# Performance work log

Hardware: AMD Instinct MI355X
Metric: run time of the kernel (lower is better)

The kernel has to match this reference:

```python
import jax, jax.numpy as jnp
import numpy as np

B, A, S, IN, H, OUT, T = 32768, 10, 50, 6, 64, 2, 60


def _p(key, shape, scale=0.1):
    return (jax.random.normal(key, shape) * scale).astype(jnp.float32)


def setup_inputs() -> dict:
    key = jax.random.key(0)
    ks = jax.random.split(key, 20)
    inp = {
        'history': jax.random.normal(ks[0], (B, A, S, IN), dtype=jnp.float32),
        # encoder layer 0 (IN->H) and layer 1 (H->H); PyTorch gate order i,f,g,o
        'enc_Wih0': _p(ks[1], (4 * H, IN)), 'enc_Whh0': _p(ks[2], (4 * H, H)),
        'enc_bih0': _p(ks[3], (4 * H,)),    'enc_bhh0': _p(ks[4], (4 * H,)),
        'enc_Wih1': _p(ks[5], (4 * H, H)),  'enc_Whh1': _p(ks[6], (4 * H, H)),
        'enc_bih1': _p(ks[7], (4 * H,)),    'enc_bhh1': _p(ks[8], (4 * H,)),
        # decoder layer 0 (OUT->H) and layer 1 (H->H)
        'dec_Wih0': _p(ks[9], (4 * H, OUT)), 'dec_Whh0': _p(ks[10], (4 * H, H)),
        'dec_bih0': _p(ks[11], (4 * H,)),    'dec_bhh0': _p(ks[12], (4 * H,)),
        'dec_Wih1': _p(ks[13], (4 * H, H)),  'dec_Whh1': _p(ks[14], (4 * H, H)),
        'dec_bih1': _p(ks[15], (4 * H,)),    'dec_bhh1': _p(ks[16], (4 * H,)),
        'lin_W': _p(ks[17], (OUT, H)), 'lin_b': _p(ks[18], (OUT,)),
        'start_token': _p(ks[19], (1, 1, OUT)),
    }
    return inp


def _cell(x, h, c, Wih, Whh, bih, bhh):
    g = x @ Wih.T + h @ Whh.T + (bih + bhh)
    i, f, gg, o = jnp.split(g, 4, axis=-1)
    c2 = jax.nn.sigmoid(f) * c + jax.nn.sigmoid(i) * jnp.tanh(gg)
    h2 = jax.nn.sigmoid(o) * jnp.tanh(c2)
    return h2, c2


def reference(history, enc_Wih0, enc_Whh0, enc_bih0, enc_bhh0,
              enc_Wih1, enc_Whh1, enc_bih1, enc_bhh1,
              dec_Wih0, dec_Whh0, dec_bih0, dec_bhh0,
              dec_Wih1, dec_Whh1, dec_bih1, dec_bhh1,
              lin_W, lin_b, start_token):
    ego = history[:, 0]                     # [B, S, IN]
    b = ego.shape[0]
    z = jnp.zeros((b, H), dtype=ego.dtype)

    def enc_step(carry, xt):
        h0, c0, h1, c1 = carry
        h0, c0 = _cell(xt, h0, c0, enc_Wih0, enc_Whh0, enc_bih0, enc_bhh0)
        h1, c1 = _cell(h0, h1, c1, enc_Wih1, enc_Whh1, enc_bih1, enc_bhh1)
        return (h0, c0, h1, c1), None

    (h0, c0, h1, c1), _ = jax.lax.scan(enc_step, (z, z, z, z),
                                       jnp.swapaxes(ego, 0, 1))  # time-major [S,B,IN]

    start = jnp.broadcast_to(start_token[0], (b, start_token.shape[2]))  # [B, OUT]

    def dec_step(carry, _):
        h0, c0, h1, c1, inp = carry
        h0, c0 = _cell(inp, h0, c0, dec_Wih0, dec_Whh0, dec_bih0, dec_bhh0)
        h1, c1 = _cell(h0, h1, c1, dec_Wih1, dec_Whh1, dec_bih1, dec_bhh1)
        out = h1 @ lin_W.T + lin_b           # [B, OUT]
        return (h0, c0, h1, c1, out), out

    _, preds = jax.lax.scan(dec_step, (h0, c0, h1, c1, start), None, length=T)
    return jnp.swapaxes(preds, 0, 1)         # [B, T, OUT]
```

## Files before the change

kernel.cpp:

```cpp
#include <hip/hip_runtime.h>
#include <stdint.h>

typedef float f32x4 __attribute__((ext_vector_type(4)));
typedef float f32x2 __attribute__((ext_vector_type(2)));
typedef __bf16 bf16x8 __attribute__((ext_vector_type(8)));
typedef __bf16 bf16x4 __attribute__((ext_vector_type(4)));

#define SEQ 50
#define TDEC 60

static __device__ __forceinline__ float ex2(float x){return __builtin_amdgcn_exp2f(x);}
static __device__ __forceinline__ float frcp_(float x){return __builtin_amdgcn_rcpf(x);}
static __device__ __forceinline__ __bf16 bfc(float x){return (__bf16)x;}

__global__ __launch_bounds__(256,2) void lstm_s2s(
    const float* __restrict__ hist,
    const float* __restrict__ eWih0, const float* __restrict__ eWhh0,
    const float* __restrict__ ebih0, const float* __restrict__ ebhh0,
    const float* __restrict__ eWih1, const float* __restrict__ eWhh1,
    const float* __restrict__ ebih1, const float* __restrict__ ebhh1,
    const float* __restrict__ dWih0, const float* __restrict__ dWhh0,
    const float* __restrict__ dbih0, const float* __restrict__ dbhh0,
    const float* __restrict__ dWih1, const float* __restrict__ dWhh1,
    const float* __restrict__ dbih1, const float* __restrict__ dbhh1,
    const float* __restrict__ linW, const float* __restrict__ linb,
    const float* __restrict__ stok,
    float* __restrict__ out)
{
  __shared__ __bf16 xch[SEQ*16*8];
  __shared__ __bf16 hb0[2][1024];
  __shared__ __bf16 hb1[2][1024];
  __shared__ __bf16 wx0s[4*4*17*8];
  __shared__ float  bC1[256];
  __shared__ __bf16 wlc[2*3*4*8];
  __shared__ float  obf[16*124];

  const int tid = threadIdx.x;
  const int lane = tid & 63;
  const int w = tid >> 6;
  const int c = lane & 15;
  const int q = lane >> 4;
  const int rsel = (q == 0) ? c : 16;
  const long rowbase = (long)blockIdx.x * 16;
  const float* eg = hist + rowbase * 3000;

  union { f32x4 f; bf16x8 h; } Z;
  Z.f[0]=0.f; Z.f[1]=0.f; Z.f[2]=0.f; Z.f[3]=0.f;
  const f32x4 zero4 = Z.f;
  const bf16x8 zfrag = Z.h;

  const float GS[4] = {-1.442695041f,-1.442695041f,2.885390082f,-1.442695041f};

  for (int i = tid; i < 16*300; i += 256) {
    int row = i / 300, o = i - row*300;
    int t = o / 6, k = o - t*6;
    xch[(t*16+row)*8 + k] = bfc(eg[row*3000 + o]);
  }
  for (int i = tid; i < 16*SEQ; i += 256) {
    xch[i*8+6] = (__bf16)1.0f;
    xch[i*8+7] = (__bf16)0.0f;
  }
  for (int i = tid; i < 512; i += 256) {
    ((uint32_t*)hb0[0])[i] = 0u;
    ((uint32_t*)hb1[0])[i] = 0u;
  }

  auto stageWx0 = [&](const float* W, int Kin, const float* bi, const float* bh) {
    for (int i = tid; i < 272; i += 256) {
      int w2 = i / 68, rem = i - w2*68;
      int g = rem / 17, row = rem - g*17;
      __bf16* dst = wx0s + i*8;
      if (row < 16) {
        int gate = (g*4 + w2)*16 + row;
        float gs = (g==2) ? 2.885390082f : -1.442695041f;
        for (int j = 0; j < 8; ++j) {
          float v = 0.f;
          if (j < Kin) v = W[gate*Kin + j];
          else if (j == 6) v = bi[gate] + bh[gate];
          dst[j] = bfc(gs*v);
        }
      } else {
        for (int j = 0; j < 8; ++j) dst[j] = (__bf16)0.f;
      }
    }
  };
  auto stageBc1 = [&](const float* bi, const float* bh) {
    for (int i = tid; i < 256; i += 256) {
      int w2 = i >> 6, g = (i >> 4) & 3, q2 = (i >> 2) & 3, r = i & 3;
      int gate = (g*4 + w2)*16 + q2*4 + r;
      float gs = (g==2) ? 2.885390082f : -1.442695041f;
      bC1[i] = gs*(bi[gate] + bh[gate]);
    }
  };

  bf16x8 whL0[4][2], wxL1[4][2], whL1[4][2];
  auto loadFull = [&](const float* W, bf16x8 (*dst)[2]) {
#pragma unroll
    for (int g = 0; g < 4; ++g)
#pragma unroll
      for (int kc = 0; kc < 2; ++kc) {
        const float* p = W + ((g*4 + w)*16 + c)*64 + kc*32 + q*8;
        f32x4 a = *(const f32x4*)p;
        f32x4 b = *(const f32x4*)(p + 4);
        bf16x8 f;
        f[0]=bfc(GS[g]*a[0]); f[1]=bfc(GS[g]*a[1]);
        f[2]=bfc(GS[g]*a[2]); f[3]=bfc(GS[g]*a[3]);
        f[4]=bfc(GS[g]*b[0]); f[5]=bfc(GS[g]*b[1]);
        f[6]=bfc(GS[g]*b[2]); f[7]=bfc(GS[g]*b[3]);
        dst[g][kc] = f;
      }
  };

  const int wconst = (w>>1)*512 + (((w&1)<<1) | (q>>1))*128 + c*8 + (q&1)*4;

  float cs0[4], cs1[4];
#pragma unroll
  for (int i = 0; i < 4; ++i) { cs0[i] = 0.f; cs1[i] = 0.f; }

  auto epilogue = [&](f32x4* a, float* cs, __bf16* hnxt) {
    bf16x4 hv;
#pragma unroll
    for (int r = 0; r < 4; ++r) {
      float eI = ex2(a[0][r]);
      float eF = ex2(a[1][r]);
      float eG = ex2(a[2][r]);
      float eO = ex2(a[3][r]);
      float P  = (1.f+eI)*(eG+1.f);
      float tt = 1.f+eF;
      float D  = frcp_(tt*P);
      float c2 = (cs[r]*P + (eG-1.f)*tt)*D;
      float eC = ex2(2.885390082f*c2);
      float h2 = (eC-1.f)*frcp_((1.f+eO)*(eC+1.f));
      cs[r] = c2;
      hv[r] = bfc(h2);
    }
    *(bf16x4*)(hnxt + wconst) = hv;
  };

  stageWx0(eWih0, 6, ebih0, ebhh0);
  stageBc1(ebih1, ebhh1);
  loadFull(eWhh0, whL0);
  loadFull(eWih1, wxL1);
  loadFull(eWhh1, whL1);
  __syncthreads();

  f32x4 acc0[4];
  {
    bf16x8 xf = zfrag;
    if (q == 0) xf = *(const bf16x8*)(xch + c*8);
#pragma unroll
    for (int g = 0; g < 4; ++g) {
      bf16x8 wxf = *(const bf16x8*)(wx0s + ((w*4+g)*17 + rsel)*8);
      acc0[g] = __builtin_amdgcn_mfma_f32_16x16x32_bf16(wxf, xf, zero4, 0,0,0);
    }
  }

  int pc = 0;
#pragma unroll 1
  for (int t = 0; t < SEQ; ++t) {
    f32x4 acc1[4];
    {
      const __bf16* h1p = hb1[pc];
      bf16x8 hf0 = *(const bf16x8*)(h1p + lane*8);
      bf16x8 hf1 = *(const bf16x8*)(h1p + 512 + lane*8);
#pragma unroll
      for (int g = 0; g < 4; ++g) {
        f32x4 bi4 = *(const f32x4*)(bC1 + w*64 + g*16 + q*4);
        acc1[g] = __builtin_amdgcn_mfma_f32_16x16x32_bf16(whL1[g][0], hf0, bi4, 0,0,0);
      }
#pragma unroll
      for (int g = 0; g < 4; ++g)
        acc1[g] = __builtin_amdgcn_mfma_f32_16x16x32_bf16(whL1[g][1], hf1, acc1[g], 0,0,0);
    }
    epilogue(acc0, cs0, hb0[pc^1]);
    __syncthreads();
    {
      const __bf16* h0n = hb0[pc^1];
      bf16x8 xf0 = *(const bf16x8*)(h0n + lane*8);
      bf16x8 xf1 = *(const bf16x8*)(h0n + 512 + lane*8);
#pragma unroll
      for (int g = 0; g < 4; ++g)
        acc1[g] = __builtin_amdgcn_mfma_f32_16x16x32_bf16(wxL1[g][0], xf0, acc1[g], 0,0,0);
#pragma unroll
      for (int g = 0; g < 4; ++g)
        acc1[g] = __builtin_amdgcn_mfma_f32_16x16x32_bf16(wxL1[g][1], xf1, acc1[g], 0,0,0);
      epilogue(acc1, cs1, hb1[pc^1]);
      if (t + 1 < SEQ) {
        bf16x8 xf = zfrag;
        if (q == 0) xf = *(const bf16x8*)(xch + (t+1)*128 + c*8);
#pragma unroll
        for (int g = 0; g < 4; ++g) {
          bf16x8 wxf = *(const bf16x8*)(wx0s + ((w*4+g)*17 + rsel)*8);
          acc0[g] = __builtin_amdgcn_mfma_f32_16x16x32_bf16(wxf, xf, zero4, 0,0,0);
        }
#pragma unroll
        for (int g = 0; g < 4; ++g)
          acc0[g] = __builtin_amdgcn_mfma_f32_16x16x32_bf16(whL0[g][0], xf0, acc0[g], 0,0,0);
#pragma unroll
        for (int g = 0; g < 4; ++g)
          acc0[g] = __builtin_amdgcn_mfma_f32_16x16x32_bf16(whL0[g][1], xf1, acc0[g], 0,0,0);
      }
    }
    __syncthreads();
    pc ^= 1;
  }

  stageWx0(dWih0, 2, dbih0, dbhh0);
  stageBc1(dbih1, dbhh1);
  loadFull(dWhh0, whL0);
  loadFull(dWih1, wxL1);
  loadFull(dWhh1, whL1);
  for (int i = tid; i < 24; i += 256) {
    int kc = i / 12, rem = i - kc*12;
    int row = rem / 4, q2 = rem - row*4;
    __bf16* dst = wlc + i*8;
    for (int j = 0; j < 8; ++j)
      dst[j] = (row < 2) ? bfc(linW[row*64 + kc*32 + q2*8 + j]) : (__bf16)0.f;
  }
  const float lb0 = linb[0], lb1 = linb[1];
  const float s0 = stok[0], s1 = stok[1];
  __syncthreads();

  bf16x8 xdec = zfrag;
  if (q == 0) { xdec[0] = bfc(s0); xdec[1] = bfc(s1); xdec[6] = (__bf16)1.0f; }
  {
    const __bf16* h0p = hb0[pc];
    bf16x8 hf0 = *(const bf16x8*)(h0p + lane*8);
    bf16x8 hf1 = *(const bf16x8*)(h0p + 512 + lane*8);
#pragma unroll
    for (int g = 0; g < 4; ++g) {
      bf16x8 wxf = *(const bf16x8*)(wx0s + ((w*4+g)*17 + rsel)*8);
      acc0[g] = __builtin_amdgcn_mfma_f32_16x16x32_bf16(wxf, xdec, zero4, 0,0,0);
    }
#pragma unroll
    for (int g = 0; g < 4; ++g)
      acc0[g] = __builtin_amdgcn_mfma_f32_16x16x32_bf16(whL0[g][0], hf0, acc0[g], 0,0,0);
#pragma unroll
    for (int g = 0; g < 4; ++g)
      acc0[g] = __builtin_amdgcn_mfma_f32_16x16x32_bf16(whL0[g][1], hf1, acc0[g], 0,0,0);
  }

#pragma unroll 1
  for (int t = 0; t < TDEC; ++t) {
    f32x4 acc1[4];
    {
      const __bf16* h1p = hb1[pc];
      bf16x8 hf0 = *(const bf16x8*)(h1p + lane*8);
      bf16x8 hf1 = *(const bf16x8*)(h1p + 512 + lane*8);
#pragma unroll
      for (int g = 0; g < 4; ++g) {
        f32x4 bi4 = *(const f32x4*)(bC1 + w*64 + g*16 + q*4);
        acc1[g] = __builtin_amdgcn_mfma_f32_16x16x32_bf16(whL1[g][0], hf0, bi4, 0,0,0);
      }
#pragma unroll
      for (int g = 0; g < 4; ++g)
        acc1[g] = __builtin_amdgcn_mfma_f32_16x16x32_bf16(whL1[g][1], hf1, acc1[g], 0,0,0);
    }
    epilogue(acc0, cs0, hb0[pc^1]);
    __syncthreads();
    {
      const __bf16* h0n = hb0[pc^1];
      bf16x8 xf0 = *(const bf16x8*)(h0n + lane*8);
      bf16x8 xf1 = *(const bf16x8*)(h0n + 512 + lane*8);
#pragma unroll
      for (int g = 0; g < 4; ++g)
        acc1[g] = __builtin_amdgcn_mfma_f32_16x16x32_bf16(wxL1[g][0], xf0, acc1[g], 0,0,0);
#pragma unroll
      for (int g = 0; g < 4; ++g)
        acc1[g] = __builtin_amdgcn_mfma_f32_16x16x32_bf16(wxL1[g][1], xf1, acc1[g], 0,0,0);
      epilogue(acc1, cs1, hb1[pc^1]);
      if (t + 1 < TDEC) {
#pragma unroll
        for (int g = 0; g < 4; ++g)
          acc0[g] = __builtin_amdgcn_mfma_f32_16x16x32_bf16(whL0[g][0], xf0, zero4, 0,0,0);
#pragma unroll
        for (int g = 0; g < 4; ++g)
          acc0[g] = __builtin_amdgcn_mfma_f32_16x16x32_bf16(whL0[g][1], xf1, acc0[g], 0,0,0);
      }
    }
    __syncthreads();
    {
      const __bf16* h1n = hb1[pc^1];
      bf16x8 xh0 = *(const bf16x8*)(h1n + lane*8);
      bf16x8 xh1 = *(const bf16x8*)(h1n + 512 + lane*8);
      int hr = (c < 2) ? c : 2;
      bf16x8 wl0 = *(const bf16x8*)(wlc + hr*32 + q*8);
      bf16x8 wl1 = *(const bf16x8*)(wlc + 96 + hr*32 + q*8);
      f32x4 oa = __builtin_amdgcn_mfma_f32_16x16x32_bf16(wl0, xh0, zero4, 0,0,0);
      oa = __builtin_amdgcn_mfma_f32_16x16x32_bf16(wl1, xh1, oa, 0,0,0);
      if (q == 0) {
        float v0 = oa[0] + lb0, v1 = oa[1] + lb1;
        if (w == 0) {
          f32x2 vv; vv[0] = v0; vv[1] = v1;
          *(f32x2*)(obf + c*124 + t*2) = vv;
        }
        xdec[0] = bfc(v0); xdec[1] = bfc(v1);
      }
      if (t + 1 < TDEC) {
#pragma unroll
        for (int g = 0; g < 4; ++g) {
          bf16x8 wxf = *(const bf16x8*)(wx0s + ((w*4+g)*17 + rsel)*8);
          acc0[g] = __builtin_amdgcn_mfma_f32_16x16x32_bf16(wxf, xdec, acc0[g], 0,0,0);
        }
      }
    }
    pc ^= 1;
  }

  __syncthreads();
  for (int i = tid; i < 480; i += 256) {
    int row = i / 30;
    int j = (i - row*30) * 4;
    f32x4 v = *(const f32x4*)(obf + row*124 + j);
    *(f32x4*)(out + rowbase*120 + i*4) = v;
  }
}

extern "C" void kernel_launch(void* const* d_in, const int* in_sizes, int n_in,
                              void* d_out, int out_size, void* d_ws, size_t ws_size,
                              hipStream_t stream) {
  (void)in_sizes; (void)n_in; (void)d_ws; (void)ws_size; (void)out_size;
  const float* p[20];
  for (int i = 0; i < 20; ++i) p[i] = (const float*)d_in[i];
  dim3 grid(2048), block(256);
  hipLaunchKernelGGL(lstm_s2s, grid, block, 0, stream,
                     p[0], p[1], p[2], p[3], p[4], p[5], p[6], p[7], p[8], p[9],
                     p[10], p[11], p[12], p[13], p[14], p[15], p[16], p[17], p[18], p[19],
                     (float*)d_out);
}
```

Baseline: 1.069 ms.

## Process two 16-row batch groups per block to amortize weights and barriers

Each block now handles 32 batch rows as two interleaved 16-row groups, with doubled hidden-state buffers and per-group accumulators and cell states. The register-resident weight fragments and each __syncthreads are shared across both groups, and the two independent MFMA chains give more instruction-level parallelism on the serial recurrence. The grid is halved and the output staging buffer now aliases the input staging area. In exchange, register pressure roughly doubles for accumulators, which risks spills at launch bounds of 2 blocks per CU, and there are fewer blocks to hide latency.

After: 1.020 ms. 1.05x faster.

```diff
diff --git a/kernel.cpp b/kernel.cpp
--- a/kernel.cpp
+++ b/kernel.cpp
@@ -27,13 +27,12 @@
     const float* __restrict__ stok,
     float* __restrict__ out)
 {
-  __shared__ __bf16 xch[SEQ*16*8];
-  __shared__ __bf16 hb0[2][1024];
-  __shared__ __bf16 hb1[2][1024];
+  __shared__ __bf16 xch[SEQ*32*8];
+  __shared__ __bf16 hb0[2][2][1024];
+  __shared__ __bf16 hb1[2][2][1024];
   __shared__ __bf16 wx0s[4*4*17*8];
   __shared__ float  bC1[256];
   __shared__ __bf16 wlc[2*3*4*8];
-  __shared__ float  obf[16*124];
 
   const int tid = threadIdx.x;
   const int lane = tid & 63;
@@ -41,7 +40,7 @@
   const int c = lane & 15;
   const int q = lane >> 4;
   const int rsel = (q == 0) ? c : 16;
-  const long rowbase = (long)blockIdx.x * 16;
+  const long rowbase = (long)blockIdx.x * 32;
   const float* eg = hist + rowbase * 3000;
 
   union { f32x4 f; bf16x8 h; } Z;
@@ -51,16 +50,16 @@
 
   const float GS[4] = {-1.442695041f,-1.442695041f,2.885390082f,-1.442695041f};
 
-  for (int i = tid; i < 16*300; i += 256) {
+  for (int i = tid; i < 32*300; i += 256) {
     int row = i / 300, o = i - row*300;
     int t = o / 6, k = o - t*6;
-    xch[(t*16+row)*8 + k] = bfc(eg[row*3000 + o]);
-  }
-  for (int i = tid; i < 16*SEQ; i += 256) {
+    xch[(t*32+row)*8 + k] = bfc(eg[row*3000 + o]);
+  }
+  for (int i = tid; i < 32*SEQ; i += 256) {
     xch[i*8+6] = (__bf16)1.0f;
     xch[i*8+7] = (__bf16)0.0f;
   }
-  for (int i = tid; i < 512; i += 256) {
+  for (int i = tid; i < 1024; i += 256) {
     ((uint32_t*)hb0[0])[i] = 0u;
     ((uint32_t*)hb1[0])[i] = 0u;
   }
@@ -113,9 +112,11 @@
 
   const int wconst = (w>>1)*512 + (((w&1)<<1) | (q>>1))*128 + c*8 + (q&1)*4;
 
-  float cs0[4], cs1[4];
-#pragma unroll
-  for (int i = 0; i < 4; ++i) { cs0[i] = 0.f; cs1[i] = 0.f; }
+  float cs0[2][4], cs1[2][4];
+#pragma unroll
+  for (int gp = 0; gp < 2; ++gp)
+#pragma unroll
+    for (int i = 0; i < 4; ++i) { cs0[gp][i] = 0.f; cs1[gp][i] = 0.f; }
 
   auto epilogue = [&](f32x4* a, float* cs, __bf16* hnxt) {
     bf16x4 hv;
@@ -144,61 +145,75 @@
   loadFull(eWhh1, whL1);
   __syncthreads();
 
-  f32x4 acc0[4];
-  {
+  f32x4 acc0[2][4];
+#pragma unroll
+  for (int gp = 0; gp < 2; ++gp) {
     bf16x8 xf = zfrag;
-    if (q == 0) xf = *(const bf16x8*)(xch + c*8);
+    if (q == 0) xf = *(const bf16x8*)(xch + gp*128 + c*8);
 #pragma unroll
     for (int g = 0; g < 4; ++g) {
       bf16x8 wxf = *(const bf16x8*)(wx0s + ((w*4+g)*17 + rsel)*8);
-      acc0[g] = __builtin_amdgcn_mfma_f32_16x16x32_bf16(wxf, xf, zero4, 0,0,0);
+      acc0[gp][g] = __builtin_amdgcn_mfma_f32_16x16x32_bf16(wxf, xf, zero4, 0,0,0);
     }
   }
 
   int pc = 0;
 #pragma unroll 1
   for (int t = 0; t < SEQ; ++t) {
-    f32x4 acc1[4];
-    {
-      const __bf16* h1p = hb1[pc];
+    f32x4 acc1[2][4];
+#pragma unroll
+    for (int gp = 0; gp < 2; ++gp) {
+      const __bf16* h1p = hb1[pc][gp];
       bf16x8 hf0 = *(const bf16x8*)(h1p + lane*8);
       bf16x8 hf1 = *(const bf16x8*)(h1p + 512 + lane*8);
 #pragma unroll
       for (int g = 0; g < 4; ++g) {
         f32x4 bi4 = *(const f32x4*)(bC1 + w*64 + g*16 + q*4);
-        acc1[g] = __builtin_amdgcn_mfma_f32_16x16x32_bf16(whL1[g][0], hf0, bi4, 0,0,0);
-      }
-#pragma unroll
-      for (int g = 0; g < 4; ++g)
-        acc1[g] = __builtin_amdgcn_mfma_f32_16x16x32_bf16(whL1[g][1], hf1, acc1[g], 0,0,0);
-    }
-    epilogue(acc0, cs0, hb0[pc^1]);
+        acc1[gp][g] = __builtin_amdgcn_mfma_f32_16x16x32_bf16(whL1[g][0], hf0, bi4, 0,0,0);
+      }
+#pragma unroll
+      for (int g = 0; g < 4; ++g)
+        acc1[gp][g] = __builtin_amdgcn_mfma_f32_16x16x32_bf16(whL1[g][1], hf1, acc1[gp][g], 0,0,0);
+    }
+#pragma unroll
+    for (int gp = 0; gp < 2; ++gp)
+      epilogue(acc0[gp], cs0[gp], hb0[pc^1][gp]);
     __syncthreads();
-    {
-      const __bf16* h0n = hb0[pc^1];
-      bf16x8 xf0 = *(const bf16x8*)(h0n + lane*8);
-      bf16x8 xf1 = *(const bf16x8*)(h0n + 512 + lane*8);
-#pragma unroll
-      for (int g = 0; g < 4; ++g)
-        acc1[g] = __builtin_amdgcn_mfma_f32_16x16x32_bf16(wxL1[g][0], xf0, acc1[g], 0,0,0);
-#pragma unroll
-      for (int g = 0; g < 4; ++g)
-        acc1[g] = __builtin_amdgcn_mfma_f32_16x16x32_bf16(wxL1[g][1], xf1, acc1[g], 0,0,0);
-      epilogue(acc1, cs1, hb1[pc^1]);
-      if (t + 1 < SEQ) {
+    bf16x8 xf0[2], xf1[2];
+#pragma unroll
+    for (int gp = 0; gp < 2; ++gp) {
+      const __bf16* h0n = hb0[pc^1][gp];
+      xf0[gp] = *(const bf16x8*)(h0n + lane*8);
+      xf1[gp] = *(const bf16x8*)(h0n + 512 + lane*8);
+    }
+#pragma unroll
+    for (int gp = 0; gp < 2; ++gp) {
+#pragma unroll
+      for (int g = 0; g < 4; ++g)
+        acc1[gp][g] = __builtin_amdgcn_mfma_f32_16x16x32_bf16(wxL1[g][0], xf0[gp], acc1[gp][g], 0,0,0);
+#pragma unroll
+      for (int g = 0; g < 4; ++g)
+        acc1[gp][g] = __builtin_amdgcn_mfma_f32_16x16x32_bf16(wxL1[g][1], xf1[gp], acc1[gp][g], 0,0,0);
+    }
+#pragma unroll
+    for (int gp = 0; gp < 2; ++gp)
+      epilogue(acc1[gp], cs1[gp], hb1[pc^1][gp]);
+    if (t + 1 < SEQ) {
+#pragma unroll
+      for (int gp = 0; gp < 2; ++gp) {
         bf16x8 xf = zfrag;
-        if (q == 0) xf = *(const bf16x8*)(xch + (t+1)*128 + c*8);
+        if (q == 0) xf = *(const bf16x8*)(xch + (t+1)*256 + gp*128 + c*8);
 #pragma unroll
         for (int g = 0; g < 4; ++g) {
           bf16x8 wxf = *(const bf16x8*)(wx0s + ((w*4+g)*17 + rsel)*8);
-          acc0[g] = __builtin_amdgcn_mfma_f32_16x16x32_bf16(wxf, xf, zero4, 0,0,0);
+          acc0[gp][g] = __builtin_amdgcn_mfma_f32_16x16x32_bf16(wxf, xf, zero4, 0,0,0);
         }
 #pragma unroll
         for (int g = 0; g < 4; ++g)
-          acc0[g] = __builtin_amdgcn_mfma_f32_16x16x32_bf16(whL0[g][0], xf0, acc0[g], 0,0,0);
+          acc0[gp][g] = __builtin_amdgcn_mfma_f32_16x16x32_bf16(whL0[g][0], xf0[gp], acc0[gp][g], 0,0,0);
 #pragma unroll
         for (int g = 0; g < 4; ++g)
-          acc0[g] = __builtin_amdgcn_mfma_f32_16x16x32_bf16(whL0[g][1], xf1, acc0[g], 0,0,0);
+          acc0[gp][g] = __builtin_amdgcn_mfma_f32_16x16x32_bf16(whL0[g][1], xf1[gp], acc0[gp][g], 0,0,0);
       }
     }
     __syncthreads();
@@ -221,66 +236,86 @@
   const float s0 = stok[0], s1 = stok[1];
   __syncthreads();
 
-  bf16x8 xdec = zfrag;
-  if (q == 0) { xdec[0] = bfc(s0); xdec[1] = bfc(s1); xdec[6] = (__bf16)1.0f; }
-  {
-    const __bf16* h0p = hb0[pc];
+  float* obf = (float*)xch;
+  bf16x8 xdec[2];
+#pragma unroll
+  for (int gp = 0; gp < 2; ++gp) {
+    xdec[gp] = zfrag;
+    if (q == 0) { xdec[gp][0] = bfc(s0); xdec[gp][1] = bfc(s1); xdec[gp][6] = (__bf16)1.0f; }
+  }
+#pragma unroll
+  for (int gp = 0; gp < 2; ++gp) {
+    const __bf16* h0p = hb0[pc][gp];
     bf16x8 hf0 = *(const bf16x8*)(h0p + lane*8);
     bf16x8 hf1 = *(const bf16x8*)(h0p + 512 + lane*8);
 #pragma unroll
     for (int g = 0; g < 4; ++g) {
       bf16x8 wxf = *(const bf16x8*)(wx0s + ((w*4+g)*17 + rsel)*8);
-      acc0[g] = __builtin_amdgcn_mfma_f32_16x16x32_bf16(wxf, xdec, zero4, 0,0,0);
+      acc0[gp][g] = __builtin_amdgcn_mfma_f32_16x16x32_bf16(wxf, xdec[gp], zero4, 0,0,0);
     }
 #pragma unroll
     for (int g = 0; g < 4; ++g)
-      acc0[g] = __builtin_amdgcn_mfma_f32_16x16x32_bf16(whL0[g][0], hf0, acc0[g], 0,0,0);
+      acc0[gp][g] = __builtin_amdgcn_mfma_f32_16x16x32_bf16(whL0[g][0], hf0, acc0[gp][g], 0,0,0);
 #pragma unroll
     for (int g = 0; g < 4; ++g)
-      acc0[g] = __builtin_amdgcn_mfma_f32_16x16x32_bf16(whL0[g][1], hf1, acc0[g], 0,0,0);
+      acc0[gp][g] = __builtin_amdgcn_mfma_f32_16x16x32_bf16(whL0[g][1], hf1, acc0[gp][g], 0,0,0);
   }
 
 #pragma unroll 1
   for (int t = 0; t < TDEC; ++t) {
-    f32x4 acc1[4];
-    {
-      const __bf16* h1p = hb1[pc];
+    f32x4 acc1[2][4];
+#pragma unroll
+    for (int gp = 0; gp < 2; ++gp) {
+      const __bf16* h1p = hb1[pc][gp];
       bf16x8 hf0 = *(const bf16x8*)(h1p + lane*8);
       bf16x8 hf1 = *(const bf16x8*)(h1p + 512 + lane*8);
 #pragma unroll
       for (int g = 0; g < 4; ++g) {
         f32x4 bi4 = *(const f32x4*)(bC1 + w*64 + g*16 + q*4);
-        acc1[g] = __builtin_amdgcn_mfma_f32_16x16x32_bf16(whL1[g][0], hf0, bi4, 0,0,0);
-      }
-#pragma unroll
-      for (int g = 0; g < 4; ++g)
-        acc1[g] = __builtin_amdgcn_mfma_f32_16x16x32_bf16(whL1[g][1], hf1, acc1[g], 0,0,0);
-    }
-    epilogue(acc0, cs0, hb0[pc^1]);
+        acc1[gp][g] = __builtin_amdgcn_mfma_f32_16x16x32_bf16(whL1[g][0], hf0, bi4, 0,0,0);
+      }
+#pragma unroll
+      for (int g = 0; g < 4; ++g)
+        acc1[gp][g] = __builtin_amdgcn_mfma_f32_16x16x32_bf16(whL1[g][1], hf1, acc1[gp][g], 0,0,0);
+    }
+#pragma unroll
+    for (int gp = 0; gp < 2; ++gp)
+      epilogue(acc0[gp], cs0[gp], hb0[pc^1][gp]);
     __syncthreads();
-    {
-      const __bf16* h0n = hb0[pc^1];
-      bf16x8 xf0 = *(const bf16x8*)(h0n + lane*8);
-      bf16x8 xf1 = *(const bf16x8*)(h0n + 512 + lane*8);
-#pragma unroll
-      for (int g = 0; g < 4; ++g)
-        acc1[g] = __builtin_amdgcn_mfma_f32_16x16x32_bf16(wxL1[g][0], xf0, acc1[g], 0,0,0);
-#pragma unroll
-      for (int g = 0; g < 4; ++g)
-        acc1[g] = __builtin_amdgcn_mfma_f32_16x16x32_bf16(wxL1[g][1], xf1, acc1[g], 0,0,0);
-      epilogue(acc1, cs1, hb1[pc^1]);
-      if (t + 1 < TDEC) {
+    bf16x8 xf0[2], xf1[2];
+#pragma unroll
+    for (int gp = 0; gp < 2; ++gp) {
+      const __bf16* h0n = hb0[pc^1][gp];
+      xf0[gp] = *(const bf16x8*)(h0n + lane*8);
+      xf1[gp] = *(const bf16x8*)(h0n + 512 + lane*8);
+    }
+#pragma unroll
+    for (int gp = 0; gp < 2; ++gp) {
+#pragma unroll
+      for (int g = 0; g < 4; ++g)
+        acc1[gp][g] = __builtin_amdgcn_mfma_f32_16x16x32_bf16(wxL1[g][0], xf0[gp], acc1[gp][g], 0,0,0);
+#pragma unroll
+      for (int g = 0; g < 4; ++g)
+        acc1[gp][g] = __builtin_amdgcn_mfma_f32_16x16x32_bf16(wxL1[g][1], xf1[gp], acc1[gp][g], 0,0,0);
+    }
+#pragma unroll
+    for (int gp = 0; gp < 2; ++gp)
+      epilogue(acc1[gp], cs1[gp], hb1[pc^1][gp]);
+    if (t + 1 < TDEC) {
+#pragma unroll
+      for (int gp = 0; gp < 2; ++gp) {
 #pragma unroll
         for (int g = 0; g < 4; ++g)
-          acc0[g] = __builtin_amdgcn_mfma_f32_16x16x32_bf16(whL0[g][0], xf0, zero4, 0,0,0);
+          acc0[gp][g] = __builtin_amdgcn_mfma_f32_16x16x32_bf16(whL0[g][0], xf0[gp], zero4, 0,0,0);
 #pragma unroll
         for (int g = 0; g < 4; ++g)
-          acc0[g] = __builtin_amdgcn_mfma_f32_16x16x32_bf16(whL0[g][1], xf1, acc0[g], 0,0,0);
+          acc0[gp][g] = __builtin_amdgcn_mfma_f32_16x16x32_bf16(whL0[g][1], xf1[gp], acc0[gp][g], 0,0,0);
       }
     }
     __syncthreads();
-    {
-      const __bf16* h1n = hb1[pc^1];
+#pragma unroll
+    for (int gp = 0; gp < 2; ++gp) {
+      const __bf16* h1n = hb1[pc^1][gp];
       bf16x8 xh0 = *(const bf16x8*)(h1n + lane*8);
       bf16x8 xh1 = *(const bf16x8*)(h1n + 512 + lane*8);
       int hr = (c < 2) ? c : 2;
@@ -292,23 +327,25 @@
         float v0 = oa[0] + lb0, v1 = oa[1] + lb1;
         if (w == 0) {
           f32x2 vv; vv[0] = v0; vv[1] = v1;
-          *(f32x2*)(obf + c*124 + t*2) = vv;
+          *(f32x2*)(obf + (gp*16+c)*124 + t*2) = vv;
         }
-        xdec[0] = bfc(v0); xdec[1] = bfc(v1);
-      }
-      if (t + 1 < TDEC) {
+        xdec[gp][0] = bfc(v0); xdec[gp][1] = bfc(v1);
+      }
+    }
+    if (t + 1 < TDEC) {
+#pragma unroll
+      for (int gp = 0; gp < 2; ++gp)
 #pragma unroll
         for (int g = 0; g < 4; ++g) {
           bf16x8 wxf = *(const bf16x8*)(wx0s + ((w*4+g)*17 + rsel)*8);
-          acc0[g] = __builtin_amdgcn_mfma_f32_16x16x32_bf16(wxf, xdec, acc0[g], 0,0,0);
+          acc0[gp][g] = __builtin_amdgcn_mfma_f32_16x16x32_bf16(wxf, xdec[gp], acc0[gp][g], 0,0,0);
         }
-      }
     }
     pc ^= 1;
   }
 
   __syncthreads();
-  for (int i = tid; i < 480; i += 256) {
+  for (int i = tid; i < 960; i += 256) {
     int row = i / 30;
     int j = (i - row*30) * 4;
     f32x4 v = *(const f32x4*)(obf + row*124 + j);
@@ -322,7 +359,7 @@
   (void)in_sizes; (void)n_in; (void)d_ws; (void)ws_size; (void)out_size;
   const float* p[20];
   for (int i = 0; i < 20; ++i) p[i] = (const float*)d_in[i];
-  dim3 grid(2048), block(256);
+  dim3 grid(1024), block(256);
   hipLaunchKernelGGL(lstm_s2s, grid, block, 0, stream,
                      p[0], p[1], p[2], p[3], p[4], p[5], p[6], p[7], p[8], p[9],
                      p[10], p[11], p[12], p[13], p[14], p[15], p[16], p[17], p[18], p[19],
```
